# Performance work log

Hardware: AMD Instinct MI355X
Metric: run time of the kernel (lower is better)

The kernel has to match this reference:

```python
import jax, jax.numpy as jnp
import numpy as np

B, F, S = 8, 4000, 512   # batch, input_size, seq_len
E = H = 128              # embedding_size == hidden_size (linearlist applied to embedded nodes)
TOPK = 8
USE_MASK = True
EPS = 1e-4


def setup_inputs() -> dict:
    key = jax.random.key(0)
    k1, k2, k3, k4, k5 = jax.random.split(key, 5)
    be = 1.0 / np.sqrt(E)
    bh = 1.0 / np.sqrt(H)
    inputs = jax.random.uniform(k1, (B, F, S), dtype=jnp.float32)
    embedding = jax.random.uniform(k2, (F, E), minval=-be, maxval=be, dtype=jnp.float32)
    # stacked nn.ModuleList of seq_len Linear(hidden_size, seq_len) layers
    W = jax.random.uniform(k3, (S, H, S), minval=-bh, maxval=bh, dtype=jnp.float32)
    b = jax.random.uniform(k4, (S, S), minval=-bh, maxval=bh, dtype=jnp.float32)
    offset_prob = jax.random.uniform(k5, (1,), dtype=jnp.float32)  # unused by forward
    return {"inputs": inputs, "embedding": embedding, "W": W, "b": b, "offset_prob": offset_prob}


def _probs(inputs, embedding, W, b):
    # GraphEmbedding: tanh(inputs[:, :, i]^T @ embedding) for each node i -> [B,S,E]
    embedded = jnp.tanh(jnp.einsum('bfs,fe->bse', inputs, embedding))
    # per-node linear: logits[b, i, :] = embedded[b, i, :] @ W[i] + b[i]
    logits = jnp.einsum('bih,iho->bio', embedded, W) + b[None]
    return jnp.clip(jax.nn.sigmoid(logits), EPS, 1.0 - EPS)  # [B,S,S], == prev_probs


def _select_and_mask(probs):
    """Sequential per-node edge sampling + acyclic (transitive-closure) mask update.

    mask[b, a, c] == True  <=>  a is an ancestor of c in the DAG built so far.
    Vectorized equivalent of compute_mask/mask propagation in the torch source.
    """
    keys = jax.random.split(jax.random.key(42), S)
    batch_ix = jnp.arange(B)[:, None]

    def step(mask, xs):
        idx, key, p = xs  # p: [B, S] probabilities for node idx's parents
        samp = jax.random.bernoulli(key, p)  # [B, S] bool
        if TOPK != 0:
            _, top_ids = jax.lax.top_k(p, TOPK)
            keep = jnp.zeros((B, S), bool).at[batch_ix, top_ids].set(True)
            samp = samp & keep
        if USE_MASK:
            # apply_mask_to_actions: cannot pick a descendant of idx as parent
            samp = samp & ~mask[:, idx, :]
        samp = samp.at[:, idx].set(False)  # no self loop
        if USE_MASK:
            # compute_mask: add edges j->idx for selected j, keep transitive closure
            anc_of_sel = jnp.any(mask & samp[:, None, :], axis=-1)   # ancestors of any selected j
            col = mask[:, :, idx] | samp | anc_of_sel                # new ancestors of idx
            mask = mask.at[:, :, idx].set(col)
            row = mask[:, idx, :]                                    # descendants of idx
            mask = mask | (col[:, :, None] & row[:, None, :])        # anc(idx) x desc(idx)
        return mask, samp

    mask0 = jnp.zeros((B, S, S), bool)
    p_steps = jnp.transpose(probs, (1, 0, 2))  # [S, B, S]
    mask, rows = jax.lax.scan(step, mask0, (jnp.arange(S), keys, p_steps))
    prev_idxs = jnp.transpose(rows, (1, 0, 2))  # [B, S, S]
    return prev_idxs, mask


def reference(inputs, embedding, W, b, offset_prob):
    prev_probs = _probs(inputs, embedding, W, b)
    prev_idxs, mask = _select_and_mask(prev_probs)
    prev_probs_2 = jnp.zeros_like(prev_probs)  # never written in the torch forward
    return prev_probs, prev_probs_2, prev_idxs, mask
```

## Files before the change

### kernel.cpp

```cpp
#include <hip/hip_runtime.h>
#include <stdint.h>

#define S_    512
#define B_    8
#define F_    4000
#define E_    128
#define H_    128
#define TOPK_ 8
#define S2_   (S_*S_)
#define BSS_  (B_*S2_)
#define BSE_  (B_*S_*E_)
#define NCHUNK_ 8
typedef unsigned long long ull;

__device__ __forceinline__ void tf2x32(uint32_t k0, uint32_t k1, uint32_t& x0, uint32_t& x1) {
  uint32_t k2 = k0 ^ k1 ^ 0x1BD11BDAu;
  x0 += k0; x1 += k1;
#define TFR(r) { x0 += x1; x1 = (x1 << (r)) | (x1 >> (32 - (r))); x1 ^= x0; }
  TFR(13) TFR(15) TFR(26) TFR(6)
  x0 += k1; x1 += k2 + 1u;
  TFR(17) TFR(29) TFR(16) TFR(24)
  x0 += k2; x1 += k0 + 2u;
  TFR(13) TFR(15) TFR(26) TFR(6)
  x0 += k0; x1 += k1 + 3u;
  TFR(17) TFR(29) TFR(16) TFR(24)
  x0 += k1; x1 += k2 + 4u;
  TFR(13) TFR(15) TFR(26) TFR(6)
  x0 += k2; x1 += k0 + 5u;
#undef TFR
}

__device__ __forceinline__ void splitkey(int i, uint32_t& k0, uint32_t& k1) {
  uint32_t x0 = 0u, x1 = (uint32_t)i;
  tf2x32(0u, 42u, x0, x1);
  k0 = x0; k1 = x1;
}
__device__ __forceinline__ uint32_t randbits32(uint32_t k0, uint32_t k1, uint32_t m) {
  uint32_t x0 = 0u, x1 = m;
  tf2x32(k0, k1, x0, x1);
  return x0 ^ x1;
}

__global__ __launch_bounds__(256) void embed_kernel(const float* __restrict__ inputs,
                                                    const float* __restrict__ embedding,
                                                    double* __restrict__ part) {
  const int c  = blockIdx.x >> 7;
  const int b  = (blockIdx.x >> 4) & 7;
  const int s0 = (blockIdx.x & 15) << 5;
  const int fbeg = c << 9;
  const int fend = (fbeg + 512 < F_) ? fbeg + 512 : F_;
  const int t  = threadIdx.x;
  const int sl = t >> 4;
  const int eg = t & 15;
  __shared__ float inA[16][32];
  double acc0[8], acc1[8];
#pragma unroll
  for (int j = 0; j < 8; j++) { acc0[j] = 0.0; acc1[j] = 0.0; }
  const int lr = t >> 4, lc = t & 15;
  const float* ip = inputs + (size_t)(b*F_ + fbeg + lr)*S_ + s0 + lc;
  float r0 = ip[0], r1 = ip[16];
  for (int f0 = fbeg; f0 < fend; f0 += 16) {
    __syncthreads();
    inA[lr][lc]      = r0;
    inA[lr][lc + 16] = r1;
    __syncthreads();
    if (f0 + 16 < fend) {
      ip += (size_t)16*S_;
      r0 = ip[0]; r1 = ip[16];
    }
#pragma unroll
    for (int k = 0; k < 16; k++) {
      double a0 = (double)inA[k][sl];
      double a1 = (double)inA[k][sl + 16];
      const float4* ep = (const float4*)(embedding + (size_t)(f0 + k)*E_ + eg*8);
      float4 w0 = ep[0], w1 = ep[1];
      double wd0 = (double)w0.x, wd1 = (double)w0.y, wd2 = (double)w0.z, wd3 = (double)w0.w;
      double wd4 = (double)w1.x, wd5 = (double)w1.y, wd6 = (double)w1.z, wd7 = (double)w1.w;
      acc0[0] += a0*wd0; acc0[1] += a0*wd1; acc0[2] += a0*wd2; acc0[3] += a0*wd3;
      acc0[4] += a0*wd4; acc0[5] += a0*wd5; acc0[6] += a0*wd6; acc0[7] += a0*wd7;
      acc1[0] += a1*wd0; acc1[1] += a1*wd1; acc1[2] += a1*wd2; acc1[3] += a1*wd3;
      acc1[4] += a1*wd4; acc1[5] += a1*wd5; acc1[6] += a1*wd6; acc1[7] += a1*wd7;
    }
  }
  double* op0 = part + (size_t)c*BSE_ + (size_t)(b*S_ + s0 + sl)*E_ + eg*8;
  double* op1 = op0 + 16*E_;
#pragma unroll
  for (int j = 0; j < 8; j++) { op0[j] = acc0[j]; op1[j] = acc1[j]; }
}

__global__ __launch_bounds__(256) void reduce_tanh_kernel(float* __restrict__ outbase) {
  const size_t j = (size_t)blockIdx.x*256 + threadIdx.x;
  const double* part = (const double*)outbase;
  double s = 0.0;
#pragma unroll
  for (int c = 0; c < NCHUNK_; c++) s += part[(size_t)c*BSE_ + j];
  double* emb64 = (double*)(outbase + 3*(size_t)BSS_);
  emb64[j] = tanh(s);
}

__global__ __launch_bounds__(256) void logits_kernel(const double* __restrict__ emb64,
                                                     const float* __restrict__ W,
                                                     const float* __restrict__ bias,
                                                     double* __restrict__ p64,
                                                     float* __restrict__ p32) {
  const int i  = blockIdx.x >> 3;
  const int o0 = (blockIdx.x & 7) << 6;
  const int t  = threadIdx.x;
  const int o  = o0 + (t & 63);
  const int bg = t >> 6;
  __shared__ double eL[8][128];
#pragma unroll
  for (int k = 0; k < 4; k++) {
    int q = t + k*256;
    eL[q >> 7][q & 127] = emb64[(size_t)((q >> 7)*S_ + i)*E_ + (q & 127)];
  }
  __syncthreads();
  double a0 = 0.0, a1 = 0.0;
  const float* Wp = W + (size_t)i*H_*S_ + o;
  for (int h = 0; h < H_; h++) {
    double w = (double)Wp[(size_t)h*S_];
    a0 += eL[bg][h]     * w;
    a1 += eL[bg + 4][h] * w;
  }
  double bd = (double)bias[i*S_ + o];
  double q0 = 1.0 / (1.0 + exp(-(a0 + bd)));
  double q1 = 1.0 / (1.0 + exp(-(a1 + bd)));
  q0 = fmin(fmax(q0, 1e-4), 1.0 - 1e-4);
  q1 = fmin(fmax(q1, 1e-4), 1.0 - 1e-4);
  size_t i0 = (size_t)(bg*S_ + i)*S_ + o;
  size_t i1 = (size_t)((bg + 4)*S_ + i)*S_ + o;
  p64[i0] = q0; p64[i1] = q1;
  p32[i0] = (float)q0; p32[i1] = (float)q1;
}

__global__ __launch_bounds__(64) void samppre_kernel(const double* __restrict__ p64,
                                                     float* __restrict__ outbase) {
  const int i = blockIdx.x >> 3;
  const int b = blockIdx.x & 7;
  const int l = threadIdx.x;
  ull* samp_pre = (ull*)(outbase + 3*(size_t)BSS_ + (size_t)b*S2_);
  uint32_t k0, k1;
  splitkey(i, k0, k1);
  double pv[8]; bool sb[8]; bool usedk[8]; bool keep[8];
#pragma unroll
  for (int w = 0; w < 8; w++) {
    int c = (w << 6) + l;
    uint32_t m = (uint32_t)(b*S_ + c);
    uint32_t bits = randbits32(k0, k1, m);
    float uf = __uint_as_float((bits >> 9) | 0x3f800000u) - 1.0f;
    double p = p64[(size_t)(b*S_ + i)*S_ + c];
    pv[w] = p;
    sb[w] = ((double)uf < p) && (c != i);
    usedk[w] = false; keep[w] = false;
  }
  for (int r = 0; r < TOPK_; r++) {
    double bp = -1.0; int bc = 0x7fffffff;
#pragma unroll
    for (int w = 0; w < 8; w++) {
      int c = (w << 6) + l;
      if (!usedk[w] && (pv[w] > bp || (pv[w] == bp && c < bc))) { bp = pv[w]; bc = c; }
    }
#pragma unroll
    for (int d = 1; d < 64; d <<= 1) {
      double op = __shfl_xor(bp, d);
      int    oc = __shfl_xor(bc, d);
      if (op > bp || (op == bp && oc < bc)) { bp = op; bc = oc; }
    }
    if ((bc & 63) == l) { usedk[bc >> 6] = true; keep[bc >> 6] = true; }
  }
#pragma unroll
  for (int w = 0; w < 8; w++) {
    ull word = __ballot((int)(sb[w] && keep[w]));
    if (l == 0) samp_pre[i*8 + w] = word;
  }
}

__global__ __launch_bounds__(512, 1) void scan_kernel(float* __restrict__ outbase) {
  const int b  = blockIdx.x;
  const int wv = threadIdx.x >> 6;
  const int l  = threadIdx.x & 63;
  const ull* __restrict__ samp_pre = (const ull*)(outbase + 3*(size_t)BSS_ + (size_t)b*S2_);
  ull* sampPack = (ull*)(outbase + (size_t)BSS_) + (size_t)b*8192;
  ull* Dpack    = sampPack + 4096;

  __shared__ ull spreL[4096];
  __shared__ ull rowbuf[2][8];
  for (int q = threadIdx.x; q < 4096; q += 512) spreL[q] = samp_pre[q];
  if (threadIdx.x < 16) ((ull*)rowbuf)[threadIdx.x] = 0ULL;
  ull Dw[8];
#pragma unroll
  for (int w = 0; w < 8; w++) Dw[w] = 0ULL;
  __syncthreads();

#pragma unroll
  for (int iw = 0; iw < 8; iw++) {
    for (int ib = 0; ib < 64; ib++) {
      const int idx  = (iw << 6) + ib;
      const int nidx = (idx + 1) & (S_ - 1);
      const int niw  = nidx >> 6, nib = nidx & 63;
      ull row[8];
#pragma unroll
      for (int w = 0; w < 8; w++) row[w] = rowbuf[idx & 1][w];
      const ull row_v = rowbuf[idx & 1][wv];
      const ull pre_v = spreL[(idx << 3) + wv];
      ull sw[8];
#pragma unroll
      for (int w = 0; w < 8; w++) sw[w] = spreL[(idx << 3) + w] & ~row[w];
      const ull swv = pre_v & ~row_v;
      const ull ibit = 1ULL << ib;
      ull t = Dw[iw] & ibit;
#pragma unroll
      for (int w = 0; w < 8; w++) {
        if (sw[w] != 0ULL) t |= Dw[w] & sw[w];
      }
      const ull col = __ballot((int)(t != 0ULL)) | swv;
      if (col != 0ULL) {
        const ull m = 0ULL - ((col >> l) & 1ULL);
        Dw[iw] |= (row[iw] | ibit) & m;
#pragma unroll
        for (int w = 0; w < 8; w++) {
          if (w != iw && row[w] != 0ULL) Dw[w] |= row[w] & m;
        }
      }
      if (wv == niw && l == nib) {
#pragma unroll
        for (int w = 0; w < 8; w++) rowbuf[nidx & 1][w] = Dw[w];
      }
      if (wv == 0) {
        ull myw = sw[0];
#pragma unroll
        for (int w = 1; w < 8; w++) myw = (l == w) ? sw[w] : myw;
        if (l < 8) sampPack[(idx << 3) + l] = myw;
      }
      __syncthreads();
    }
  }
#pragma unroll
  for (int w = 0; w < 8; w++)
    Dpack[(((wv << 3) + w) << 6) + l] = Dw[w];
}

__global__ __launch_bounds__(256) void expand_kernel(float* __restrict__ outbase) {
  const ull* pack = (const ull*)(outbase + (size_t)BSS_);
  unsigned int tid = blockIdx.x*256 + threadIdx.x;
  const unsigned int half = 1u << 18;
  if (tid < half) {
    unsigned int t = tid;
    int b = t >> 15, tin = t & 32767, r = tin >> 6, cg = tin & 63;
    ull word = pack[(size_t)b*8192 + (r << 3) + (cg >> 3)];
    int sh = (cg & 7) << 3;
    float* dst = outbase + 2*(size_t)BSS_ + ((size_t)b << 18) + (r << 9) + (cg << 3);
    float4 v0 = make_float4((float)((word >> (sh+0)) & 1ULL), (float)((word >> (sh+1)) & 1ULL),
                            (float)((word >> (sh+2)) & 1ULL), (float)((word >> (sh+3)) & 1ULL));
    float4 v1 = make_float4((float)((word >> (sh+4)) & 1ULL), (float)((word >> (sh+5)) & 1ULL),
                            (float)((word >> (sh+6)) & 1ULL), (float)((word >> (sh+7)) & 1ULL));
    ((float4*)dst)[0] = v0; ((float4*)dst)[1] = v1;
  } else {
    unsigned int t = tid - half;
    int b = t >> 15, tin = t & 32767, a = tin >> 6, cg = tin & 63;
    const ull* Dp = pack + (size_t)b*8192 + 4096;
    ull word = Dp[((((a >> 6) << 3) + (cg >> 3)) << 6) + (a & 63)];
    int sh = (cg & 7) << 3;
    float* dst = outbase + 3*(size_t)BSS_ + ((size_t)b << 18) + (a << 9) + (cg << 3);
    float4 v0 = make_float4((float)((word >> (sh+0)) & 1ULL), (float)((word >> (sh+1)) & 1ULL),
                            (float)((word >> (sh+2)) & 1ULL), (float)((word >> (sh+3)) & 1ULL));
    float4 v1 = make_float4((float)((word >> (sh+4)) & 1ULL), (float)((word >> (sh+5)) & 1ULL),
                            (float)((word >> (sh+6)) & 1ULL), (float)((word >> (sh+7)) & 1ULL));
    ((float4*)dst)[0] = v0; ((float4*)dst)[1] = v1;
  }
}

extern "C" void kernel_launch(void* const* d_in, const int* in_sizes, int n_in,
                              void* d_out, int out_size, void* d_ws, size_t ws_size,
                              hipStream_t stream) {
  const float* inputs    = (const float*)d_in[0];
  const float* embedding = (const float*)d_in[1];
  const float* W         = (const float*)d_in[2];
  const float* bias      = (const float*)d_in[3];
  float* out = (float*)d_out;
  double* part  = (double*)out;
  double* emb64 = (double*)(out + 3*(size_t)BSS_);
  double* p64   = (double*)(out + (size_t)BSS_);

  embed_kernel      <<<1024, 256, 0, stream>>>(inputs, embedding, part);
  reduce_tanh_kernel<<<2048, 256, 0, stream>>>(out);
  logits_kernel     <<<4096, 256, 0, stream>>>(emb64, W, bias, p64, out);
  samppre_kernel    <<<4096, 64,  0, stream>>>(p64, out);
  scan_kernel       <<<8,    512, 0, stream>>>(out);
  expand_kernel     <<<2048, 256, 0, stream>>>(out);
  hipMemsetAsync(out + (size_t)BSS_, 0, (size_t)BSS_ * sizeof(float), stream);
}
```

Baseline: 517.7 us.

## Compute embedding GEMM with FP64 MFMA and runtime lane-layout probing

Replaces the shared-memory FP64 FMA tiling in the embedding GEMM with one wavefront per 16x16 output tile that uses the v_mfma_f64_16x16x4 matrix instruction. The kernel first probes the MFMA operand and result lane layout at runtime and falls back to a scalar FP64 loop if the layout is not recognised. This removes the shared-memory staging and synchronisation, but each lane now issues strided single-element global loads of inputs and embedding for every k step. The grid grows fourfold to one tile per wave.

```diff
diff --git a/kernel.cpp b/kernel.cpp
--- a/kernel.cpp
+++ b/kernel.cpp
@@ -12,6 +12,7 @@
 #define BSE_  (B_*S_*E_)
 #define NCHUNK_ 8
 typedef unsigned long long ull;
+typedef __attribute__((ext_vector_type(4))) double d4;
 
 __device__ __forceinline__ void tf2x32(uint32_t k0, uint32_t k1, uint32_t& x0, uint32_t& x1) {
   uint32_t k2 = k0 ^ k1 ^ 0x1BD11BDAu;
@@ -44,48 +45,63 @@
 __global__ __launch_bounds__(256) void embed_kernel(const float* __restrict__ inputs,
                                                     const float* __restrict__ embedding,
                                                     double* __restrict__ part) {
-  const int c  = blockIdx.x >> 7;
-  const int b  = (blockIdx.x >> 4) & 7;
-  const int s0 = (blockIdx.x & 15) << 5;
+  const int wid = blockIdx.x*4 + (threadIdx.x >> 6);
+  const int c  = wid >> 11;
+  const int b  = (wid >> 8) & 7;
+  const int s0 = ((wid >> 3) & 31) << 4;
+  const int e0 = (wid & 7) << 4;
   const int fbeg = c << 9;
   const int fend = (fbeg + 512 < F_) ? fbeg + 512 : F_;
-  const int t  = threadIdx.x;
-  const int sl = t >> 4;
-  const int eg = t & 15;
-  __shared__ float inA[16][32];
-  double acc0[8], acc1[8];
-#pragma unroll
-  for (int j = 0; j < 8; j++) { acc0[j] = 0.0; acc1[j] = 0.0; }
-  const int lr = t >> 4, lc = t & 15;
-  const float* ip = inputs + (size_t)(b*F_ + fbeg + lr)*S_ + s0 + lc;
-  float r0 = ip[0], r1 = ip[16];
-  for (int f0 = fbeg; f0 < fend; f0 += 16) {
-    __syncthreads();
-    inA[lr][lc]      = r0;
-    inA[lr][lc + 16] = r1;
-    __syncthreads();
-    if (f0 + 16 < fend) {
-      ip += (size_t)16*S_;
-      r0 = ip[0]; r1 = ip[16];
-    }
-#pragma unroll
-    for (int k = 0; k < 16; k++) {
-      double a0 = (double)inA[k][sl];
-      double a1 = (double)inA[k][sl + 16];
-      const float4* ep = (const float4*)(embedding + (size_t)(f0 + k)*E_ + eg*8);
-      float4 w0 = ep[0], w1 = ep[1];
-      double wd0 = (double)w0.x, wd1 = (double)w0.y, wd2 = (double)w0.z, wd3 = (double)w0.w;
-      double wd4 = (double)w1.x, wd5 = (double)w1.y, wd6 = (double)w1.z, wd7 = (double)w1.w;
-      acc0[0] += a0*wd0; acc0[1] += a0*wd1; acc0[2] += a0*wd2; acc0[3] += a0*wd3;
-      acc0[4] += a0*wd4; acc0[5] += a0*wd5; acc0[6] += a0*wd6; acc0[7] += a0*wd7;
-      acc1[0] += a1*wd0; acc1[1] += a1*wd1; acc1[2] += a1*wd2; acc1[3] += a1*wd3;
-      acc1[4] += a1*wd4; acc1[5] += a1*wd5; acc1[6] += a1*wd6; acc1[7] += a1*wd7;
-    }
-  }
-  double* op0 = part + (size_t)c*BSE_ + (size_t)(b*S_ + s0 + sl)*E_ + eg*8;
-  double* op1 = op0 + 16*E_;
-#pragma unroll
-  for (int j = 0; j < 8; j++) { op0[j] = acc0[j]; op1[j] = acc1[j]; }
+  const int l  = threadIdx.x & 63;
+
+  d4 z = {0.0, 0.0, 0.0, 0.0};
+  double lv = (double)l;
+  d4 p1 = __builtin_amdgcn_mfma_f64_16x16x4f64(lv, 1.0, z, 0, 0, 0);
+  d4 p2 = __builtin_amdgcn_mfma_f64_16x16x4f64(1.0, lv, z, 0, 0, 0);
+  const int sig1 = __builtin_amdgcn_readlane((int)p1[1], 0);
+  const int sig2 = __builtin_amdgcn_readlane((int)p2[0], 1);
+  const bool known = (sig1 == 100 || sig1 == 112 || sig1 == 22 || sig1 == 70) &&
+                     (sig2 == 100 || sig2 == 22);
+
+  if (known) {
+    const bool A2 = (sig1 == 22) || (sig1 == 70);
+    const bool D2 = (sig1 == 112) || (sig1 == 70);
+    const bool B2 = (sig2 == 22);
+    const int mA = A2 ? (l >> 2) : (l & 15);
+    const int kA = A2 ? (l & 3)  : (l >> 4);
+    const int nB = B2 ? (l >> 2) : (l & 15);
+    const int kB = B2 ? (l & 3)  : (l >> 4);
+    const float* Ap = inputs    + (size_t)(b*F_ + fbeg + kA)*S_ + s0 + mA;
+    const float* Bp = embedding + (size_t)(fbeg + kB)*E_ + e0 + nB;
+    d4 acc = {0.0, 0.0, 0.0, 0.0};
+    for (int f = fbeg; f < fend; f += 4) {
+      acc = __builtin_amdgcn_mfma_f64_16x16x4f64((double)Ap[0], (double)Bp[0], acc, 0, 0, 0);
+      Ap += (size_t)4*S_;
+      Bp += (size_t)4*E_;
+    }
+    const int rb = D2 ? (l >> 4) : ((l >> 4) << 2);
+    const int rs = D2 ? 4 : 1;
+    double* op = part + (size_t)c*BSE_ + (size_t)(b*S_ + s0 + rb)*E_ + e0 + (l & 15);
+    op[0]               = acc[0];
+    op[(size_t)rs*E_]   = acc[1];
+    op[(size_t)2*rs*E_] = acc[2];
+    op[(size_t)3*rs*E_] = acc[3];
+  } else {
+    const int m = l & 15, kq = l >> 4;
+    double a0 = 0.0, a1 = 0.0, a2 = 0.0, a3 = 0.0;
+    const float* ipb = inputs + (size_t)(b*F_ + fbeg)*S_ + s0 + 4*kq;
+    const float* epb = embedding + (size_t)fbeg*E_ + e0 + m;
+    for (int f = fbeg; f < fend; f++) {
+      double e = (double)epb[0];
+      a0 += (double)ipb[0] * e;
+      a1 += (double)ipb[1] * e;
+      a2 += (double)ipb[2] * e;
+      a3 += (double)ipb[3] * e;
+      ipb += S_; epb += E_;
+    }
+    double* op = part + (size_t)c*BSE_ + (size_t)(b*S_ + s0 + 4*kq)*E_ + e0 + m;
+    op[0] = a0; op[E_] = a1; op[2*E_] = a2; op[3*E_] = a3;
+  }
 }
 
 __global__ __launch_bounds__(256) void reduce_tanh_kernel(float* __restrict__ outbase) {
@@ -282,7 +298,7 @@
   double* emb64 = (double*)(out + 3*(size_t)BSS_);
   double* p64   = (double*)(out + (size_t)BSS_);
 
-  embed_kernel      <<<1024, 256, 0, stream>>>(inputs, embedding, part);
+  embed_kernel      <<<4096, 256, 0, stream>>>(inputs, embedding, part);
   reduce_tanh_kernel<<<2048, 256, 0, stream>>>(out);
   logits_kernel     <<<4096, 256, 0, stream>>>(emb64, W, bias, p64, out);
   samppre_kernel    <<<4096, 64,  0, stream>>>(p64, out);
```

Result: faster. 497.5 us (-3.9%).
